# Kernel optimization log

Hardware: AMD Instinct MI355X
Metric: run time of the kernel (lower is better)

Reference implementation:

```python
import jax, jax.numpy as jnp
import numpy as np

N = 50000
E = 800000
D = 96


def setup_inputs() -> dict:
    key = jax.random.key(0)
    ks = jax.random.split(key, 9)
    x = jax.random.normal(ks[0], (N, D), dtype=jnp.float32)
    edge_index = jax.random.randint(ks[1], (2, E), 0, N, dtype=jnp.int64)
    s = 1.0 / np.sqrt(D)
    # PyG GraphConv: lin_rel (with bias) on aggregated neighbors, lin_root (no bias) on self.
    W1_rel = jax.random.uniform(ks[2], (D, D), jnp.float32, -s, s)
    b1_rel = jax.random.uniform(ks[3], (D,), jnp.float32, -s, s)
    W1_root = jax.random.uniform(ks[4], (D, D), jnp.float32, -s, s)
    W2_rel = jax.random.uniform(ks[5], (D, D), jnp.float32, -s, s)
    b2_rel = jax.random.uniform(ks[6], (D,), jnp.float32, -s, s)
    W2_root = jax.random.uniform(ks[7], (D, D), jnp.float32, -s, s)
    return {
        "x": x, "edge_index": edge_index,
        "W1_rel": W1_rel, "b1_rel": b1_rel, "W1_root": W1_root,
        "W2_rel": W2_rel, "b2_rel": b2_rel, "W2_root": W2_root,
    }


def _graph_conv(x, src, dst, W_rel, b_rel, W_root):
    # gather source features, sum-scatter to destinations (PyG aggr='add')
    agg = jax.ops.segment_sum(x[src], dst, num_segments=N)  # [N, D]
    return agg @ W_rel + b_rel + x @ W_root


def reference(x, edge_index, W1_rel, b1_rel, W1_root, W2_rel, b2_rel, W2_root):
    src, dst = edge_index[0], edge_index[1]
    h = jax.nn.relu(_graph_conv(x, src, dst, W1_rel, b1_rel, W1_root))
    out = _graph_conv(h, src, dst, W2_rel, b2_rel, W2_root)
    return out
```

## Files before the change

### kernel.cpp

```cpp
#include <hip/hip_runtime.h>
#include <hip/hip_bf16.h>

#define DD 96
#define CB_BITS 7
#define CB_SIZE 128
#define CB_MAXBINS 512
#define CBE 2048
#define BIN_CAP 4096
#define AGG_STRIDE 104

typedef __attribute__((ext_vector_type(8))) short short8;
typedef __attribute__((ext_vector_type(4))) float floatx4;

__device__ __forceinline__ int load_idx(const void* eidx, int isI64, int pos) {
    return isI64 ? (int)((const long long*)eidx)[pos] : ((const int*)eidx)[pos];
}

__device__ __forceinline__ unsigned int b16(float f) {
    unsigned int u = __float_as_uint(f);
    return (u + 0x7fffu + ((u >> 16) & 1u)) >> 16;
}
__device__ __forceinline__ unsigned int pack2(float lo, float hi) {
    return b16(lo) | (b16(hi) << 16);
}

__global__ __launch_bounds__(256) void prep_kernel(
    const float* __restrict__ x,
    const float* __restrict__ W1_rel, const float* __restrict__ W1_root,
    const float* __restrict__ W2_rel, const float* __restrict__ W2_root,
    const unsigned long long* __restrict__ idx64,
    int* __restrict__ flag, int* __restrict__ binCursor,
    unsigned short* __restrict__ xb,
    uint4* __restrict__ wpack1, uint4* __restrict__ wpack2,
    long long nelem, unsigned long long nmax, int nbins) {
    const int b = blockIdx.x;
    const int tid = threadIdx.x;
    if (b == 0) {
        __shared__ int bad;
        if (tid == 0) bad = 0;
        __syncthreads();
        unsigned long long v = idx64[tid];
        if (v >= nmax) bad = 1;
        __syncthreads();
        if (tid == 0) *flag = bad ? 0 : 1;
        for (int i = tid; i < nbins; i += 256) binCursor[i] = i * BIN_CAP;
        return;
    }
    if (b <= 18) {
        int t = (b - 1) * 256 + tid;
        int layer = t / 2304;
        int tt = t - layer * 2304;
        const float* Wr = layer ? W2_rel : W1_rel;
        const float* Wo = layer ? W2_root : W1_root;
        uint4* wp = layer ? wpack2 : wpack1;
        int f = tt >> 6, lane = tt & 63;
        int kt = f / 6, nt = f % 6;
        int n = nt * 16 + (lane & 15);
        int kbase = kt * 32 + (lane >> 4) * 8;
        float v[8];
        #pragma unroll
        for (int j = 0; j < 8; ++j) {
            int k = kbase + j;
            v[j] = (k < DD) ? Wr[(size_t)k * DD + n]
                            : Wo[(size_t)(k - DD) * DD + n];
        }
        uint4 o;
        o.x = pack2(v[0], v[1]); o.y = pack2(v[2], v[3]);
        o.z = pack2(v[4], v[5]); o.w = pack2(v[6], v[7]);
        wp[tt] = o;
        return;
    }
    long long i = ((long long)(b - 19) * 256 + tid) * 8;
    if (i + 8 > nelem) return;
    float4 f0 = ((const float4*)(x + i))[0];
    float4 f1 = ((const float4*)(x + i))[1];
    uint4 o;
    o.x = pack2(f0.x, f0.y); o.y = pack2(f0.z, f0.w);
    o.z = pack2(f1.x, f1.y); o.w = pack2(f1.z, f1.w);
    *((uint4*)(xb + i)) = o;
}

__global__ __launch_bounds__(256) void coarse_bin_kernel(
    const void* __restrict__ eidx, const int* __restrict__ flag,
    int* __restrict__ binCursor, uint2* __restrict__ estage,
    int E, int n, int nbins) {
    __shared__ int cnt[CB_MAXBINS];
    __shared__ int pref[CB_MAXBINS];
    __shared__ int cur[CB_MAXBINS];
    __shared__ int gbase[CB_MAXBINS];
    __shared__ uint2 ebuf[CBE];
    __shared__ int tot_sh;
    const int tid = threadIdx.x;
    for (int i = tid; i < CB_MAXBINS; i += 256) cnt[i] = 0;
    __syncthreads();
    const int base = blockIdx.x * CBE;
    const int isI64 = *flag;
    int sr[8], dr[8];
    #pragma unroll
    for (int i = 0; i < 8; ++i) {
        int e = base + tid + i * 256;
        sr[i] = -1; dr[i] = -1;
        if (e < E) {
            int s = load_idx(eidx, isI64, e);
            int d = load_idx(eidx, isI64, E + e);
            if ((unsigned)s < (unsigned)n && (unsigned)d < (unsigned)n) {
                sr[i] = s; dr[i] = d;
                atomicAdd(&cnt[d >> CB_BITS], 1);
            }
        }
    }
    __syncthreads();
    {
        int a0 = cnt[2 * tid], a1 = cnt[2 * tid + 1];
        int ps = a0 + a1;
        gbase[tid] = ps;
        __syncthreads();
        int v = ps;
        for (int off = 1; off < 256; off <<= 1) {
            int o = (tid >= off) ? gbase[tid - off] : 0;
            __syncthreads();
            v += o;
            gbase[tid] = v;
            __syncthreads();
        }
        int ex = v - ps;
        pref[2 * tid] = ex;      pref[2 * tid + 1] = ex + a0;
        cur[2 * tid]  = ex;      cur[2 * tid + 1]  = ex + a0;
        if (tid == 255) tot_sh = v;
    }
    __syncthreads();
    const int tot = tot_sh;
    #pragma unroll
    for (int i = 0; i < 8; ++i) {
        if (dr[i] >= 0) {
            int r = atomicAdd(&cur[dr[i] >> CB_BITS], 1);
            ebuf[r] = make_uint2((unsigned)sr[i], (unsigned)dr[i]);
        }
    }
    __syncthreads();
    for (int i = tid; i < nbins; i += 256) {
        int c = cnt[i];
        gbase[i] = c ? atomicAdd(&binCursor[i], c) : 0;
    }
    __syncthreads();
    for (int k = tid; k < tot; k += 256) {
        uint2 e = ebuf[k];
        int bin = (int)(e.y >> CB_BITS);
        int g = gbase[bin] + (k - pref[bin]);
        if (g < (bin + 1) * BIN_CAP) estage[g] = e;
    }
}

__device__ __forceinline__ void acc8(float* a, uint4 w) {
    a[0] += __uint_as_float(w.x << 16); a[1] += __uint_as_float(w.x & 0xffff0000u);
    a[2] += __uint_as_float(w.y << 16); a[3] += __uint_as_float(w.y & 0xffff0000u);
    a[4] += __uint_as_float(w.z << 16); a[5] += __uint_as_float(w.z & 0xffff0000u);
    a[6] += __uint_as_float(w.w << 16); a[7] += __uint_as_float(w.w & 0xffff0000u);
}

__global__ __launch_bounds__(512) void layer_kernel(
    const uint2* __restrict__ estage, const int* __restrict__ binCursor,
    const unsigned short* __restrict__ feat, const uint4* __restrict__ wpack,
    const float* __restrict__ bias, float* __restrict__ outf,
    unsigned short* __restrict__ outb, int n, int do_relu) {
    __shared__ int cnt[CB_SIZE];
    __shared__ int stl[CB_SIZE];
    __shared__ int cur[CB_SIZE];
    __shared__ int pref[CB_SIZE];
    __shared__ int ssrc_l[BIN_CAP];
    __shared__ unsigned short agg_l[CB_SIZE * AGG_STRIDE];
    const int b = blockIdx.x;
    const int tid = threadIdx.x;
    const uint2* ebin = estage + (size_t)b * BIN_CAP;
    int tot = binCursor[b] - b * BIN_CAP;
    tot = (tot < 0) ? 0 : (tot > BIN_CAP ? BIN_CAP : tot);
    if (tid < CB_SIZE) cnt[tid] = 0;
    __syncthreads();
    for (int k = tid; k < tot; k += 512)
        atomicAdd(&cnt[ebin[k].y & (CB_SIZE - 1)], 1);
    __syncthreads();
    {
        int v = (tid < CB_SIZE) ? cnt[tid] : 0;
        if (tid < CB_SIZE) pref[tid] = v;
        __syncthreads();
        for (int off = 1; off < CB_SIZE; off <<= 1) {
            int o = (tid < CB_SIZE && tid >= off) ? pref[tid - off] : 0;
            __syncthreads();
            if (tid < CB_SIZE) { v += o; pref[tid] = v; }
            __syncthreads();
        }
        if (tid < CB_SIZE) {
            int st = v - cnt[tid];
            stl[tid] = st;
            cur[tid] = st;
        }
    }
    __syncthreads();
    for (int k = tid; k < tot; k += 512) {
        uint2 e = ebin[k];
        int pos = atomicAdd(&cur[e.y & (CB_SIZE - 1)], 1);
        ssrc_l[pos] = (int)e.x;
    }
    __syncthreads();
    #pragma unroll
    for (int it = 0; it < 3; ++it) {
        int p = it * 512 + tid;
        int nl = p / 12, c = p % 12;
        int node = (b << CB_BITS) + nl;
        float accA[8] = {0,0,0,0,0,0,0,0};
        float accB[8] = {0,0,0,0,0,0,0,0};
        if (node < n) {
            int st = stl[nl], en = st + cnt[nl];
            int j = st;
            for (; j + 4 <= en; j += 4) {
                int s0 = ssrc_l[j + 0], s1 = ssrc_l[j + 1];
                int s2 = ssrc_l[j + 2], s3 = ssrc_l[j + 3];
                uint4 w0 = ((const uint4*)(feat + (size_t)s0 * DD))[c];
                uint4 w1 = ((const uint4*)(feat + (size_t)s1 * DD))[c];
                uint4 w2 = ((const uint4*)(feat + (size_t)s2 * DD))[c];
                uint4 w3 = ((const uint4*)(feat + (size_t)s3 * DD))[c];
                acc8(accA, w0); acc8(accB, w1); acc8(accA, w2); acc8(accB, w3);
            }
            for (; j < en; ++j) {
                uint4 w = ((const uint4*)(feat + (size_t)ssrc_l[j] * DD))[c];
                acc8(accA, w);
            }
        }
        uint4 o;
        o.x = pack2(accA[0] + accB[0], accA[1] + accB[1]);
        o.y = pack2(accA[2] + accB[2], accA[3] + accB[3]);
        o.z = pack2(accA[4] + accB[4], accA[5] + accB[5]);
        o.w = pack2(accA[6] + accB[6], accA[7] + accB[7]);
        *((uint4*)&agg_l[nl * AGG_STRIDE + c * 8]) = o;
    }
    __syncthreads();
    {
        const int lane = tid & 63;
        const int w = tid >> 6;
        const int p = w >> 2;
        const int mt0 = w & 3;
        const int m16 = lane & 15;
        const int quad = lane >> 4;
        const int rowbase = b << CB_BITS;

        short8 bfrag[6][3];
        #pragma unroll
        for (int kt = 0; kt < 6; ++kt)
            #pragma unroll
            for (int ntl = 0; ntl < 3; ++ntl) {
                uint4 u = wpack[(kt * 6 + (p * 3 + ntl)) * 64 + lane];
                bfrag[kt][ntl] = *(short8*)&u;
            }

        floatx4 acc[2][3];
        #pragma unroll
        for (int mi = 0; mi < 2; ++mi)
            #pragma unroll
            for (int ntl = 0; ntl < 3; ++ntl)
                acc[mi][ntl] = (floatx4){0.f, 0.f, 0.f, 0.f};

        #pragma unroll
        for (int kt = 0; kt < 6; ++kt) {
            short8 afrag[2];
            #pragma unroll
            for (int mi = 0; mi < 2; ++mi) {
                const int mt = mt0 + mi * 4;
                const int mrow = mt * 16 + m16;
                if (kt < 3) {
                    afrag[mi] = *(const short8*)
                        &agg_l[mrow * AGG_STRIDE + kt * 32 + quad * 8];
                } else {
                    int row = rowbase + mrow;
                    int r = (row < n) ? row : 0;
                    afrag[mi] = *(const short8*)
                        (feat + (size_t)r * DD + (kt - 3) * 32 + quad * 8);
                }
            }
            #pragma unroll
            for (int ntl = 0; ntl < 3; ++ntl) {
                acc[0][ntl] = __builtin_amdgcn_mfma_f32_16x16x32_bf16(
                    afrag[0], bfrag[kt][ntl], acc[0][ntl], 0, 0, 0);
                acc[1][ntl] = __builtin_amdgcn_mfma_f32_16x16x32_bf16(
                    afrag[1], bfrag[kt][ntl], acc[1][ntl], 0, 0, 0);
            }
        }

        #pragma unroll
        for (int ntl = 0; ntl < 3; ++ntl) {
            const int col = (p * 3 + ntl) * 16 + m16;
            const float bv = bias[col];
            #pragma unroll
            for (int mi = 0; mi < 2; ++mi) {
                const int mt = mt0 + mi * 4;
                #pragma unroll
                for (int reg = 0; reg < 4; ++reg) {
                    int row = rowbase + mt * 16 + quad * 4 + reg;
                    if (row < n) {
                        float v = acc[mi][ntl][reg] + bv;
                        if (do_relu) v = fmaxf(v, 0.f);
                        if (outf) outf[(size_t)row * DD + col] = v;
                        if (outb) outb[(size_t)row * DD + col] =
                            (unsigned short)b16(v);
                    }
                }
            }
        }
    }
}

__global__ void detect_idx_kernel(const unsigned long long* __restrict__ idx,
                                  int* __restrict__ flag,
                                  unsigned long long nmax) {
    __shared__ int bad;
    if (threadIdx.x == 0) bad = 0;
    __syncthreads();
    unsigned long long v = idx[threadIdx.x];
    if (v >= nmax) bad = 1;
    __syncthreads();
    if (threadIdx.x == 0) *flag = bad ? 0 : 1;
}

__global__ __launch_bounds__(256) void scatter_add_kernel(
    const float* __restrict__ feat, const void* __restrict__ eidx,
    const int* __restrict__ flag, float* __restrict__ agg,
    int E, int n) {
    long long t = (long long)blockIdx.x * 256 + threadIdx.x;
    if (t >= (long long)E * 24) return;
    int e = (int)(t / 24);
    int c = (int)(t % 24);
    int isI64 = *flag;
    int s = load_idx(eidx, isI64, e);
    int d = load_idx(eidx, isI64, E + e);
    if ((unsigned)s >= (unsigned)n || (unsigned)d >= (unsigned)n) return;
    const float4 v = ((const float4*)(feat + (size_t)s * DD))[c];
    float* o = agg + (size_t)d * DD + (size_t)c * 4;
    atomicAdd(o + 0, v.x);
    atomicAdd(o + 1, v.y);
    atomicAdd(o + 2, v.z);
    atomicAdd(o + 3, v.w);
}

__global__ __launch_bounds__(256, 4) void linear64_kernel(
    const float* __restrict__ A, const float* __restrict__ X,
    const float* __restrict__ Wrel, const float* __restrict__ bias,
    const float* __restrict__ Wroot, float* __restrict__ out,
    int n, int do_relu) {
    __shared__ float wlds[DD * DD];
    const int lane = threadIdx.x & 63;
    const int q = threadIdx.x >> 6;
    const int j0 = q * 24;
    const int node = blockIdx.x * 64 + lane;
    const bool act = (node < n);
    const int r = act ? node : 0;
    float acc[24];
    {
        const float4* bq = (const float4*)(bias + j0);
        #pragma unroll
        for (int jj = 0; jj < 6; ++jj) {
            float4 b = bq[jj];
            acc[jj*4+0] = b.x; acc[jj*4+1] = b.y;
            acc[jj*4+2] = b.z; acc[jj*4+3] = b.w;
        }
    }
    const float* srcs[2] = {A, X};
    const float* mats[2] = {Wrel, Wroot};
    for (int phase = 0; phase < 2; ++phase) {
        {
            const float4* wg = (const float4*)mats[phase];
            float4* wl = (float4*)wlds;
            #pragma unroll
            for (int i = 0; i < 9; ++i)
                wl[threadIdx.x + i * 256] = wg[threadIdx.x + i * 256];
        }
        __syncthreads();
        const float* row = srcs[phase] + (size_t)r * DD;
        for (int kk = 0; kk < DD; kk += 4) {
            float4 a4 = *(const float4*)(row + kk);
            const float av[4] = {a4.x, a4.y, a4.z, a4.w};
            #pragma unroll
            for (int u = 0; u < 4; ++u) {
                const float4* wrow = (const float4*)(&wlds[(kk + u) * DD + j0]);
                const float ka = av[u];
                #pragma unroll
                for (int jj = 0; jj < 6; ++jj) {
                    float4 ww = wrow[jj];
                    acc[jj*4+0] = fmaf(ka, ww.x, acc[jj*4+0]);
                    acc[jj*4+1] = fmaf(ka, ww.y, acc[jj*4+1]);
                    acc[jj*4+2] = fmaf(ka, ww.z, acc[jj*4+2]);
                    acc[jj*4+3] = fmaf(ka, ww.w, acc[jj*4+3]);
                }
            }
        }
        __syncthreads();
    }
    if (act) {
        float4* o = (float4*)(out + (size_t)node * DD + j0);
        #pragma unroll
        for (int jj = 0; jj < 6; ++jj) {
            float4 v = make_float4(acc[jj*4+0], acc[jj*4+1],
                                   acc[jj*4+2], acc[jj*4+3]);
            if (do_relu) {
                v.x = fmaxf(v.x, 0.f); v.y = fmaxf(v.y, 0.f);
                v.z = fmaxf(v.z, 0.f); v.w = fmaxf(v.w, 0.f);
            }
            o[jj] = v;
        }
    }
}

__global__ __launch_bounds__(256) void linear_kernel(
    const float* __restrict__ A, const float* __restrict__ X,
    const float* __restrict__ Wrel, const float* __restrict__ bias,
    const float* __restrict__ Wroot, float* __restrict__ out,
    int n, int do_relu) {
    __shared__ float wlds[DD * DD];
    const int lane = threadIdx.x & 63;
    const int q = threadIdx.x >> 6;
    const int j0 = q * 24;
    const int m0 = blockIdx.x * 128 + lane;
    const int m1 = m0 + 64;
    const bool act0 = (m0 < n), act1 = (m1 < n);
    const int r0 = act0 ? m0 : 0;
    const int r1 = act1 ? m1 : 0;
    float acc0[24], acc1[24];
    {
        const float4* bq = (const float4*)(bias + j0);
        #pragma unroll
        for (int jj = 0; jj < 6; ++jj) {
            float4 b = bq[jj];
            acc0[jj*4+0] = b.x; acc0[jj*4+1] = b.y;
            acc0[jj*4+2] = b.z; acc0[jj*4+3] = b.w;
            acc1[jj*4+0] = b.x; acc1[jj*4+1] = b.y;
            acc1[jj*4+2] = b.z; acc1[jj*4+3] = b.w;
        }
    }
    const float* srcs[2] = {A, X};
    const float* mats[2] = {Wrel, Wroot};
    for (int phase = 0; phase < 2; ++phase) {
        {
            const float4* wg = (const float4*)mats[phase];
            float4* wl = (float4*)wlds;
            #pragma unroll
            for (int i = 0; i < 9; ++i)
                wl[threadIdx.x + i * 256] = wg[threadIdx.x + i * 256];
        }
        __syncthreads();
        const float* row0 = srcs[phase] + (size_t)r0 * DD;
        const float* row1 = srcs[phase] + (size_t)r1 * DD;
        for (int kk = 0; kk < DD; kk += 4) {
            float4 a0 = *(const float4*)(row0 + kk);
            float4 a1 = *(const float4*)(row1 + kk);
            const float av0[4] = {a0.x, a0.y, a0.z, a0.w};
            const float av1[4] = {a1.x, a1.y, a1.z, a1.w};
            #pragma unroll
            for (int u = 0; u < 4; ++u) {
                const float4* wrow = (const float4*)(&wlds[(kk + u) * DD + j0]);
                const float k0 = av0[u], k1 = av1[u];
                #pragma unroll
                for (int jj = 0; jj < 6; ++jj) {
                    float4 ww = wrow[jj];
                    acc0[jj*4+0] = fmaf(k0, ww.x, acc0[jj*4+0]);
                    acc0[jj*4+1] = fmaf(k0, ww.y, acc0[jj*4+1]);
                    acc0[jj*4+2] = fmaf(k0, ww.z, acc0[jj*4+2]);
                    acc0[jj*4+3] = fmaf(k0, ww.w, acc0[jj*4+3]);
                    acc1[jj*4+0] = fmaf(k1, ww.x, acc1[jj*4+0]);
                    acc1[jj*4+1] = fmaf(k1, ww.y, acc1[jj*4+1]);
                    acc1[jj*4+2] = fmaf(k1, ww.z, acc1[jj*4+2]);
                    acc1[jj*4+3] = fmaf(k1, ww.w, acc1[jj*4+3]);
                }
            }
        }
        __syncthreads();
    }
    if (act0) {
        float4* o = (float4*)(out + (size_t)m0 * DD + j0);
        #pragma unroll
        for (int jj = 0; jj < 6; ++jj) {
            float4 v = make_float4(acc0[jj*4+0], acc0[jj*4+1],
                                   acc0[jj*4+2], acc0[jj*4+3]);
            if (do_relu) {
                v.x = fmaxf(v.x, 0.f); v.y = fmaxf(v.y, 0.f);
                v.z = fmaxf(v.z, 0.f); v.w = fmaxf(v.w, 0.f);
            }
            o[jj] = v;
        }
    }
    if (act1) {
        float4* o = (float4*)(out + (size_t)m1 * DD + j0);
        #pragma unroll
        for (int jj = 0; jj < 6; ++jj) {
            float4 v = make_float4(acc1[jj*4+0], acc1[jj*4+1],
                                   acc1[jj*4+2], acc1[jj*4+3]);
            if (do_relu) {
                v.x = fmaxf(v.x, 0.f); v.y = fmaxf(v.y, 0.f);
                v.z = fmaxf(v.z, 0.f); v.w = fmaxf(v.w, 0.f);
            }
            o[jj] = v;
        }
    }
}

extern "C" void kernel_launch(void* const* d_in, const int* in_sizes, int n_in,
                              void* d_out, int out_size, void* d_ws, size_t ws_size,
                              hipStream_t stream) {
    const float* x      = (const float*)d_in[0];
    const void*  eidx   = d_in[1];
    const float* W1_rel = (const float*)d_in[2];
    const float* b1     = (const float*)d_in[3];
    const float* W1_root= (const float*)d_in[4];
    const float* W2_rel = (const float*)d_in[5];
    const float* b2     = (const float*)d_in[6];
    const float* W2_root= (const float*)d_in[7];
    float* out = (float*)d_out;

    const int N = in_sizes[0] / DD;
    const int E = in_sizes[1] / 2;
    const int nbins = (N + CB_SIZE - 1) >> CB_BITS;
    const long long nelem = (long long)N * DD;
    char* base = (char*)d_ws;

    size_t off = 0;
    auto alloc = [&](size_t bytes) {
        size_t o = off; off = (off + bytes + 255) & ~(size_t)255; return base + o; };
    int*   flag      = (int*)  alloc(256);
    int*   binCursor = (int*)  alloc((size_t)(CB_MAXBINS + 1) * 4);
    uint2* estage    = (uint2*)alloc((size_t)nbins * BIN_CAP * 8);
    unsigned short* xb   = (unsigned short*)alloc((size_t)nelem * 2);
    unsigned short* hb   = (unsigned short*)alloc((size_t)nelem * 2);
    uint4* wpack1    = (uint4*)alloc(36 * 64 * 16);
    uint4* wpack2    = (uint4*)alloc(36 * 64 * 16);
    const bool mfma_ok = (off <= ws_size) && (nbins <= CB_MAXBINS) &&
                         (nbins > 0) && (3LL * (E / nbins) <= 2LL * BIN_CAP);

    size_t offB = 512;
    auto allocB = [&](size_t bytes) {
        size_t o = offB; offB = (offB + bytes + 255) & ~(size_t)255; return base + o; };
    float* agg = (float*)allocB((size_t)nelem * 4);
    const bool fb_ok = (offB <= ws_size);

    if (mfma_ok) {
        const int conv_blocks = (int)((nelem / 8 + 255) / 256);
        prep_kernel<<<19 + conv_blocks, 256, 0, stream>>>(
            x, W1_rel, W1_root, W2_rel, W2_root,
            (const unsigned long long*)eidx, flag, binCursor,
            xb, wpack1, wpack2, nelem, (unsigned long long)N, nbins);
        coarse_bin_kernel<<<(E + CBE - 1) / CBE, 256, 0, stream>>>(
            eidx, flag, binCursor, estage, E, N, nbins);
        layer_kernel<<<nbins, 512, 0, stream>>>(
            estage, binCursor, xb, wpack1, b1,
            (float*)nullptr, hb, N, 1);
        layer_kernel<<<nbins, 512, 0, stream>>>(
            estage, binCursor, hb, wpack2, b2,
            out, (unsigned short*)nullptr, N, 0);
    } else if (fb_ok) {
        const int scatter_blocks = (int)(((long long)E * 24 + 255) / 256);
        detect_idx_kernel<<<1, 256, 0, stream>>>(
            (const unsigned long long*)eidx, flag, (unsigned long long)N);
        hipMemsetAsync(agg, 0, (size_t)nelem * 4, stream);
        scatter_add_kernel<<<scatter_blocks, 256, 0, stream>>>(x, eidx, flag, agg, E, N);
        linear64_kernel<<<(N + 63) / 64, 256, 0, stream>>>(
            agg, x, W1_rel, b1, W1_root, out, N, 1);
        hipMemsetAsync(agg, 0, (size_t)nelem * 4, stream);
        scatter_add_kernel<<<scatter_blocks, 256, 0, stream>>>(out, eidx, flag, agg, E, N);
        linear_kernel<<<(N + 127) / 128, 256, 0, stream>>>(
            agg, out, W2_rel, b2, W2_root, out, N, 0);
    }
}
```

Before: 167.6 us.

## Halve bin size to 64 nodes and pack edges into 32-bit words

Node bins shrink from 128 to 64 nodes, giving twice as many layer_kernel blocks (about 782 instead of 391) at 256 threads each, which should fill the GPU's compute units better. Each staged edge is packed into one 32-bit word with src in the low 16 bits and dst in the high 16 bits, halving staging traffic. The layer kernel also keeps its edge words in registers instead of reading them from global memory twice. The packing requires N <= 65536, now added as a guard, and the per-bin capacity drops to 2048, so overflow is more likely with skewed degrees.

```diff
diff --git a/kernel.cpp b/kernel.cpp
--- a/kernel.cpp
+++ b/kernel.cpp
@@ -2,11 +2,11 @@
 #include <hip/hip_bf16.h>
 
 #define DD 96
-#define CB_BITS 7
-#define CB_SIZE 128
-#define CB_MAXBINS 512
+#define CB_BITS 6
+#define CB_SIZE 64
+#define CB_MAXBINS 1024
 #define CBE 2048
-#define BIN_CAP 4096
+#define BIN_CAP 2048
 #define AGG_STRIDE 104
 
 typedef __attribute__((ext_vector_type(8))) short short8;
@@ -82,16 +82,17 @@
 
 __global__ __launch_bounds__(256) void coarse_bin_kernel(
     const void* __restrict__ eidx, const int* __restrict__ flag,
-    int* __restrict__ binCursor, uint2* __restrict__ estage,
+    int* __restrict__ binCursor, unsigned int* __restrict__ estage,
     int E, int n, int nbins) {
     __shared__ int cnt[CB_MAXBINS];
     __shared__ int pref[CB_MAXBINS];
     __shared__ int cur[CB_MAXBINS];
     __shared__ int gbase[CB_MAXBINS];
-    __shared__ uint2 ebuf[CBE];
+    __shared__ unsigned int ebuf[CBE];
     __shared__ int tot_sh;
     const int tid = threadIdx.x;
-    for (int i = tid; i < CB_MAXBINS; i += 256) cnt[i] = 0;
+    #pragma unroll
+    for (int i = 0; i < 4; ++i) cnt[tid + i * 256] = 0;
     __syncthreads();
     const int base = blockIdx.x * CBE;
     const int isI64 = *flag;
@@ -111,8 +112,9 @@
     }
     __syncthreads();
     {
-        int a0 = cnt[2 * tid], a1 = cnt[2 * tid + 1];
-        int ps = a0 + a1;
+        int a[4], ps = 0;
+        #pragma unroll
+        for (int j = 0; j < 4; ++j) { a[j] = cnt[4 * tid + j]; ps += a[j]; }
         gbase[tid] = ps;
         __syncthreads();
         int v = ps;
@@ -123,9 +125,13 @@
             gbase[tid] = v;
             __syncthreads();
         }
-        int ex = v - ps;
-        pref[2 * tid] = ex;      pref[2 * tid + 1] = ex + a0;
-        cur[2 * tid]  = ex;      cur[2 * tid + 1]  = ex + a0;
+        int run = v - ps;
+        #pragma unroll
+        for (int j = 0; j < 4; ++j) {
+            pref[4 * tid + j] = run;
+            cur[4 * tid + j] = run;
+            run += a[j];
+        }
         if (tid == 255) tot_sh = v;
     }
     __syncthreads();
@@ -134,7 +140,7 @@
     for (int i = 0; i < 8; ++i) {
         if (dr[i] >= 0) {
             int r = atomicAdd(&cur[dr[i] >> CB_BITS], 1);
-            ebuf[r] = make_uint2((unsigned)sr[i], (unsigned)dr[i]);
+            ebuf[r] = ((unsigned)dr[i] << 16) | (unsigned)sr[i];
         }
     }
     __syncthreads();
@@ -144,10 +150,10 @@
     }
     __syncthreads();
     for (int k = tid; k < tot; k += 256) {
-        uint2 e = ebuf[k];
-        int bin = (int)(e.y >> CB_BITS);
+        unsigned int u = ebuf[k];
+        int bin = (int)(u >> 22);
         int g = gbase[bin] + (k - pref[bin]);
-        if (g < (bin + 1) * BIN_CAP) estage[g] = e;
+        if (g < (bin + 1) * BIN_CAP) estage[g] = u;
     }
 }
 
@@ -158,8 +164,8 @@
     a[6] += __uint_as_float(w.w << 16); a[7] += __uint_as_float(w.w & 0xffff0000u);
 }
 
-__global__ __launch_bounds__(512) void layer_kernel(
-    const uint2* __restrict__ estage, const int* __restrict__ binCursor,
+__global__ __launch_bounds__(256) void layer_kernel(
+    const unsigned int* __restrict__ estage, const int* __restrict__ binCursor,
     const unsigned short* __restrict__ feat, const uint4* __restrict__ wpack,
     const float* __restrict__ bias, float* __restrict__ outf,
     unsigned short* __restrict__ outb, int n, int do_relu) {
@@ -171,13 +177,22 @@
     __shared__ unsigned short agg_l[CB_SIZE * AGG_STRIDE];
     const int b = blockIdx.x;
     const int tid = threadIdx.x;
-    const uint2* ebin = estage + (size_t)b * BIN_CAP;
+    const unsigned int* ebin = estage + (size_t)b * BIN_CAP;
     int tot = binCursor[b] - b * BIN_CAP;
     tot = (tot < 0) ? 0 : (tot > BIN_CAP ? BIN_CAP : tot);
     if (tid < CB_SIZE) cnt[tid] = 0;
     __syncthreads();
-    for (int k = tid; k < tot; k += 512)
-        atomicAdd(&cnt[ebin[k].y & (CB_SIZE - 1)], 1);
+    unsigned int er[8];
+    #pragma unroll
+    for (int i = 0; i < 8; ++i) {
+        int k = tid + i * 256;
+        er[i] = 0xffffffffu;
+        if (k < tot) {
+            unsigned int u = ebin[k];
+            er[i] = u;
+            atomicAdd(&cnt[(u >> 16) & (CB_SIZE - 1)], 1);
+        }
+    }
     __syncthreads();
     {
         int v = (tid < CB_SIZE) ? cnt[tid] : 0;
@@ -196,15 +211,17 @@
         }
     }
     __syncthreads();
-    for (int k = tid; k < tot; k += 512) {
-        uint2 e = ebin[k];
-        int pos = atomicAdd(&cur[e.y & (CB_SIZE - 1)], 1);
-        ssrc_l[pos] = (int)e.x;
+    #pragma unroll
+    for (int i = 0; i < 8; ++i) {
+        if (er[i] != 0xffffffffu) {
+            int pos = atomicAdd(&cur[(er[i] >> 16) & (CB_SIZE - 1)], 1);
+            ssrc_l[pos] = (int)(er[i] & 0xffffu);
+        }
     }
     __syncthreads();
     #pragma unroll
     for (int it = 0; it < 3; ++it) {
-        int p = it * 512 + tid;
+        int p = it * 256 + tid;
         int nl = p / 12, c = p % 12;
         int node = (b << CB_BITS) + nl;
         float accA[8] = {0,0,0,0,0,0,0,0};
@@ -237,8 +254,8 @@
     {
         const int lane = tid & 63;
         const int w = tid >> 6;
-        const int p = w >> 2;
-        const int mt0 = w & 3;
+        const int p = w >> 1;
+        const int sub = w & 1;
         const int m16 = lane & 15;
         const int quad = lane >> 4;
         const int rowbase = b << CB_BITS;
@@ -264,7 +281,7 @@
             short8 afrag[2];
             #pragma unroll
             for (int mi = 0; mi < 2; ++mi) {
-                const int mt = mt0 + mi * 4;
+                const int mt = sub + mi * 2;
                 const int mrow = mt * 16 + m16;
                 if (kt < 3) {
                     afrag[mi] = *(const short8*)
@@ -291,7 +308,7 @@
             const float bv = bias[col];
             #pragma unroll
             for (int mi = 0; mi < 2; ++mi) {
-                const int mt = mt0 + mi * 4;
+                const int mt = sub + mi * 2;
                 #pragma unroll
                 for (int reg = 0; reg < 4; ++reg) {
                     int row = rowbase + mt * 16 + quad * 4 + reg;
@@ -524,13 +541,14 @@
         size_t o = off; off = (off + bytes + 255) & ~(size_t)255; return base + o; };
     int*   flag      = (int*)  alloc(256);
     int*   binCursor = (int*)  alloc((size_t)(CB_MAXBINS + 1) * 4);
-    uint2* estage    = (uint2*)alloc((size_t)nbins * BIN_CAP * 8);
+    unsigned int* estage = (unsigned int*)alloc((size_t)nbins * BIN_CAP * 4);
     unsigned short* xb   = (unsigned short*)alloc((size_t)nelem * 2);
     unsigned short* hb   = (unsigned short*)alloc((size_t)nelem * 2);
     uint4* wpack1    = (uint4*)alloc(36 * 64 * 16);
     uint4* wpack2    = (uint4*)alloc(36 * 64 * 16);
     const bool mfma_ok = (off <= ws_size) && (nbins <= CB_MAXBINS) &&
-                         (nbins > 0) && (3LL * (E / nbins) <= 2LL * BIN_CAP);
+                         (nbins > 0) && (N <= 65536) &&
+                         (3LL * (E / nbins) <= 2LL * BIN_CAP);
 
     size_t offB = 512;
     auto allocB = [&](size_t bytes) {
@@ -546,10 +564,10 @@
             xb, wpack1, wpack2, nelem, (unsigned long long)N, nbins);
         coarse_bin_kernel<<<(E + CBE - 1) / CBE, 256, 0, stream>>>(
             eidx, flag, binCursor, estage, E, N, nbins);
-        layer_kernel<<<nbins, 512, 0, stream>>>(
+        layer_kernel<<<nbins, 256, 0, stream>>>(
             estage, binCursor, xb, wpack1, b1,
             (float*)nullptr, hb, N, 1);
-        layer_kernel<<<nbins, 512, 0, stream>>>(
+        layer_kernel<<<nbins, 256, 0, stream>>>(
             estage, binCursor, hb, wpack2, b2,
             out, (unsigned short*)nullptr, N, 0);
     } else if (fb_ok) {
```

Result: no change. 170.2 us (+1.6%).
